# Kernel tuning notes

Hardware: AMD Instinct MI355X
Metric: run time of the kernel (lower is better)

Reference implementation:

```python
import jax, jax.numpy as jnp
import numpy as np

# Assumptions (helpers not included in source):
#  - drop_edge(A, 0.8, training) is identity at inference (training=False); we
#    implement the deterministic eval path.
#  - normalized_laplacian_tilde_matrix(A) = D~^{-1/2} (A + I) D~^{-1/2}, the
#    renormalization-trick adjacency (A_tilde = A + I, D~ = rowsum(A_tilde)).

def setup_inputs() -> dict:
    key = jax.random.key(0)
    kx, kA, kW = jax.random.split(key, 3)
    B, C, Co, T, N, K = 64, 64, 64, 32, 64, 3
    x = jax.random.normal(kx, (B, C, T, N), dtype=jnp.float32)
    A = jax.random.uniform(kA, (B, K, T, N, N), dtype=jnp.float32)
    W = jax.random.normal(kW, (Co, C), dtype=jnp.float32) * 0.02  # 1x1 conv weight
    b = jnp.zeros((Co,), dtype=jnp.float32)
    return {"x": x, "A": A, "W": W, "b": b}


def reference(x, A, W, b):
    # 1x1 Conv2d == per-position channel mixing
    x = jnp.einsum('bctn,oc->botn', x, W) + b[None, :, None, None]

    # Vectorized normalized-Laplacian-tilde over all (B, K, T) graphs at once.
    N = A.shape[-1]
    A_tilde = A + jnp.eye(N, dtype=A.dtype)            # (B,K,T,N,N)
    deg = jnp.sum(A_tilde, axis=-1)                    # (B,K,T,N)
    dinv = jax.lax.rsqrt(deg)                          # deg >= 1, safe
    A_norm = A_tilde * dinv[..., :, None] * dinv[..., None, :]

    # Per-(k,t) bmm: out[b,c,t,m] = sum_k sum_n x[b,c,t,n] * A_norm[b,k,t,n,m]
    x_out = jnp.einsum('bctn,bktnm->bctm', x, A_norm)
    return (x_out, A)
```

## Files before the change

### kernel.cpp

```cpp
#include <hip/hip_runtime.h>
#include <hip/hip_bf16.h>

typedef __attribute__((ext_vector_type(8))) short short8;
typedef __attribute__((ext_vector_type(4))) short short4v;
typedef __attribute__((ext_vector_type(4))) float f32x4;

#define Bb 64
#define Cc 64
#define Tt 32
#define Nn 64
#define Kk 3
#define PITCH 72
#define OUT_A_OFF 8388608L

__device__ __forceinline__ short f2bf(float f) {
    __hip_bfloat16 h = __float2bfloat16(f);
    return *reinterpret_cast<short*>(&h);
}

__global__ __launch_bounds__(256, 4) void ctg_kernel(
    const float* __restrict__ X,
    const float* __restrict__ A,
    const float* __restrict__ W,
    const float* __restrict__ bias,
    float* __restrict__ out)
{
    __shared__ short sW [Cc * PITCH];
    __shared__ short sXT[Nn * PITCH];
    __shared__ short sX1[Cc * PITCH];
    __shared__ short sAT[Nn * PITCH];
    __shared__ float sDinv[Nn];
    __shared__ float sB[Cc];

    const int tid = threadIdx.x;
    const int b = blockIdx.x >> 5;
    const int t = blockIdx.x & 31;
    const int l  = tid & 63;
    const int w  = tid >> 6;
    const int lr = l & 15;
    const int lq = l >> 4;

    const long xbase = (long)b * (Cc * Tt * Nn) + (long)t * Nn;

    #pragma unroll
    for (int j = 0; j < 4; ++j) {
        int q  = tid + 256 * j;
        int r  = q >> 4;
        int c0 = (q & 15) * 4;
        f32x4 wv = *(const f32x4*)(W + r * 64 + c0);
        short4v ws;
        #pragma unroll
        for (int i = 0; i < 4; ++i) ws[i] = f2bf(wv[i]);
        *(short4v*)&sW[r * PITCH + c0] = ws;
        f32x4 xv = *(const f32x4*)(X + xbase + (long)r * (Tt * Nn) + c0);
        #pragma unroll
        for (int i = 0; i < 4; ++i) sXT[(c0 + i) * PITCH + r] = f2bf(xv[i]);
    }
    if (tid < Cc) sB[tid] = bias[tid];
    __syncthreads();

    short8 aw0 = *(const short8*)&sW[(16 * w + lr) * PITCH + 8 * lq];
    short8 aw1 = *(const short8*)&sW[(16 * w + lr) * PITCH + 32 + 8 * lq];
    f32x4 acc1[4];
    #pragma unroll
    for (int nt = 0; nt < 4; ++nt) {
        acc1[nt] = (f32x4){0.f, 0.f, 0.f, 0.f};
        short8 b0 = *(const short8*)&sXT[(16 * nt + lr) * PITCH + 8 * lq];
        short8 b1 = *(const short8*)&sXT[(16 * nt + lr) * PITCH + 32 + 8 * lq];
        acc1[nt] = __builtin_amdgcn_mfma_f32_16x16x32_bf16(aw0, b0, acc1[nt], 0, 0, 0);
        acc1[nt] = __builtin_amdgcn_mfma_f32_16x16x32_bf16(aw1, b1, acc1[nt], 0, 0, 0);
    }
    #pragma unroll
    for (int nt = 0; nt < 4; ++nt)
        #pragma unroll
        for (int r = 0; r < 4; ++r) {
            int c = 16 * w + 4 * lq + r;
            sX1[c * PITCH + 16 * nt + lr] = f2bf(acc1[nt][r] + sB[c]);
        }

    f32x4 acc3[4];
    #pragma unroll
    for (int mt = 0; mt < 4; ++mt) acc3[mt] = (f32x4){0.f, 0.f, 0.f, 0.f};

    const int m0 = (tid & 15) * 4;
    const long Abase0 = (long)b * (Kk * Tt * Nn * Nn) + (long)t * (Nn * Nn);

    for (int k = 0; k < Kk; ++k) {
        __syncthreads();

        const long Ab = Abase0 + (long)k * (Tt * Nn * Nn);
        f32x4 av[4];
        #pragma unroll
        for (int e = 0; e < 4; ++e) av[e] = *(const f32x4*)(A + Ab + 4 * (tid + 256 * e));
        #pragma unroll
        for (int e = 0; e < 4; ++e) *(f32x4*)(out + OUT_A_OFF + Ab + 4 * (tid + 256 * e)) = av[e];

        float dg[4];
        #pragma unroll
        for (int e = 0; e < 4; ++e) {
            float q = av[e][0] + av[e][1] + av[e][2] + av[e][3];
            q += __shfl_xor(q, 1);
            q += __shfl_xor(q, 2);
            q += __shfl_xor(q, 4);
            q += __shfl_xor(q, 8);
            dg[e] = q;
        }
        if ((tid & 15) == 0) {
            #pragma unroll
            for (int e = 0; e < 4; ++e)
                sDinv[(tid >> 4) + 16 * e] = rsqrtf(dg[e] + 1.0f);
        }
        __syncthreads();

        float dm[4] = { sDinv[m0], sDinv[m0 + 1], sDinv[m0 + 2], sDinv[m0 + 3] };
        #pragma unroll
        for (int e = 0; e < 4; ++e) {
            int n = (tid >> 4) + 16 * e;
            float dn = sDinv[n];
            #pragma unroll
            for (int i = 0; i < 4; ++i) {
                float v = av[e][i];
                if (m0 + i == n) v += 1.0f;
                sAT[(m0 + i) * PITCH + n] = f2bf(v * dn * dm[i]);
            }
        }
        __syncthreads();

        short8 a0 = *(const short8*)&sX1[(16 * w + lr) * PITCH + 8 * lq];
        short8 a1 = *(const short8*)&sX1[(16 * w + lr) * PITCH + 32 + 8 * lq];
        #pragma unroll
        for (int mt = 0; mt < 4; ++mt) {
            short8 b0 = *(const short8*)&sAT[(16 * mt + lr) * PITCH + 8 * lq];
            short8 b1 = *(const short8*)&sAT[(16 * mt + lr) * PITCH + 32 + 8 * lq];
            acc3[mt] = __builtin_amdgcn_mfma_f32_16x16x32_bf16(a0, b0, acc3[mt], 0, 0, 0);
            acc3[mt] = __builtin_amdgcn_mfma_f32_16x16x32_bf16(a1, b1, acc3[mt], 0, 0, 0);
        }
    }

    #pragma unroll
    for (int mt = 0; mt < 4; ++mt)
        #pragma unroll
        for (int r = 0; r < 4; ++r) {
            int c = 16 * w + 4 * lq + r;
            out[xbase + (long)c * (Tt * Nn) + 16 * mt + lr] = acc3[mt][r];
        }
}

extern "C" void kernel_launch(void* const* d_in, const int* in_sizes, int n_in,
                              void* d_out, int out_size, void* d_ws, size_t ws_size,
                              hipStream_t stream) {
    const float* X    = (const float*)d_in[0];
    const float* A    = (const float*)d_in[1];
    const float* W    = (const float*)d_in[2];
    const float* bias = (const float*)d_in[3];
    float* out = (float*)d_out;
    ctg_kernel<<<dim3(Bb * Tt), dim3(256), 0, stream>>>(X, A, W, bias, out);
}
```

Before: 243.6 us.

## Prefetch next A slice, shrink shared memory for higher occupancy, use nontemporal stores

New measurement: 250.3 us. 1.03x slower.

```diff
diff --git a/kernel.cpp b/kernel.cpp
--- a/kernel.cpp
+++ b/kernel.cpp
@@ -2,7 +2,6 @@
 #include <hip/hip_bf16.h>
 
 typedef __attribute__((ext_vector_type(8))) short short8;
-typedef __attribute__((ext_vector_type(4))) short short4v;
 typedef __attribute__((ext_vector_type(4))) float f32x4;
 
 #define Bb 64
@@ -18,19 +17,16 @@
     return *reinterpret_cast<short*>(&h);
 }
 
-__global__ __launch_bounds__(256, 4) void ctg_kernel(
+__global__ __launch_bounds__(256, 8) void ctg_kernel(
     const float* __restrict__ X,
     const float* __restrict__ A,
     const float* __restrict__ W,
     const float* __restrict__ bias,
     float* __restrict__ out)
 {
-    __shared__ short sW [Cc * PITCH];
-    __shared__ short sXT[Nn * PITCH];
-    __shared__ short sX1[Cc * PITCH];
-    __shared__ short sAT[Nn * PITCH];
+    __shared__ __align__(16) short buf1[Nn * PITCH];
+    __shared__ __align__(16) short buf0[Nn * PITCH];
     __shared__ float sDinv[Nn];
-    __shared__ float sB[Cc];
 
     const int tid = threadIdx.x;
     const int b = blockIdx.x >> 5;
@@ -40,42 +36,56 @@
     const int lr = l & 15;
     const int lq = l >> 4;
 
-    const long xbase = (long)b * (Cc * Tt * Nn) + (long)t * Nn;
+    const long xbase  = (long)b * (Cc * Tt * Nn) + (long)t * Nn;
+    const long Abase0 = (long)b * (Kk * Tt * Nn * Nn) + (long)t * (Nn * Nn);
+    const float* Aptr = A + Abase0 + 4 * tid;
+
+    f32x4 av[4];
+    #pragma unroll
+    for (int e = 0; e < 4; ++e) av[e] = *(const f32x4*)(Aptr + 1024 * e);
 
     #pragma unroll
     for (int j = 0; j < 4; ++j) {
         int q  = tid + 256 * j;
         int r  = q >> 4;
         int c0 = (q & 15) * 4;
-        f32x4 wv = *(const f32x4*)(W + r * 64 + c0);
-        short4v ws;
-        #pragma unroll
-        for (int i = 0; i < 4; ++i) ws[i] = f2bf(wv[i]);
-        *(short4v*)&sW[r * PITCH + c0] = ws;
         f32x4 xv = *(const f32x4*)(X + xbase + (long)r * (Tt * Nn) + c0);
         #pragma unroll
-        for (int i = 0; i < 4; ++i) sXT[(c0 + i) * PITCH + r] = f2bf(xv[i]);
+        for (int i = 0; i < 4; ++i) buf1[(c0 + i) * PITCH + r] = f2bf(xv[i]);
     }
-    if (tid < Cc) sB[tid] = bias[tid];
+
+    const float* wrow = W + (16 * w + lr) * 64 + 8 * lq;
+    f32x4 w00 = *(const f32x4*)(wrow);
+    f32x4 w01 = *(const f32x4*)(wrow + 4);
+    f32x4 w10 = *(const f32x4*)(wrow + 32);
+    f32x4 w11 = *(const f32x4*)(wrow + 36);
+    short8 aw0, aw1;
+    #pragma unroll
+    for (int i = 0; i < 4; ++i) {
+        aw0[i] = f2bf(w00[i]); aw0[4 + i] = f2bf(w01[i]);
+        aw1[i] = f2bf(w10[i]); aw1[4 + i] = f2bf(w11[i]);
+    }
+    f32x4 bv = *(const f32x4*)(bias + 16 * w + 4 * lq);
+
     __syncthreads();
 
-    short8 aw0 = *(const short8*)&sW[(16 * w + lr) * PITCH + 8 * lq];
-    short8 aw1 = *(const short8*)&sW[(16 * w + lr) * PITCH + 32 + 8 * lq];
     f32x4 acc1[4];
     #pragma unroll
     for (int nt = 0; nt < 4; ++nt) {
         acc1[nt] = (f32x4){0.f, 0.f, 0.f, 0.f};
-        short8 b0 = *(const short8*)&sXT[(16 * nt + lr) * PITCH + 8 * lq];
-        short8 b1 = *(const short8*)&sXT[(16 * nt + lr) * PITCH + 32 + 8 * lq];
+        short8 b0 = *(const short8*)&buf1[(16 * nt + lr) * PITCH + 8 * lq];
+        short8 b1 = *(const short8*)&buf1[(16 * nt + lr) * PITCH + 32 + 8 * lq];
         acc1[nt] = __builtin_amdgcn_mfma_f32_16x16x32_bf16(aw0, b0, acc1[nt], 0, 0, 0);
         acc1[nt] = __builtin_amdgcn_mfma_f32_16x16x32_bf16(aw1, b1, acc1[nt], 0, 0, 0);
     }
+    __syncthreads();
+
     #pragma unroll
     for (int nt = 0; nt < 4; ++nt)
         #pragma unroll
         for (int r = 0; r < 4; ++r) {
             int c = 16 * w + 4 * lq + r;
-            sX1[c * PITCH + 16 * nt + lr] = f2bf(acc1[nt][r] + sB[c]);
+            buf1[c * PITCH + 16 * nt + lr] = f2bf(acc1[nt][r] + bv[r]);
         }
 
     f32x4 acc3[4];
@@ -83,19 +93,15 @@
     for (int mt = 0; mt < 4; ++mt) acc3[mt] = (f32x4){0.f, 0.f, 0.f, 0.f};
 
     const int m0 = (tid & 15) * 4;
-    const long Abase0 = (long)b * (Kk * Tt * Nn * Nn) + (long)t * (Nn * Nn);
+    const int nrow = tid >> 4;
 
     for (int k = 0; k < Kk; ++k) {
-        __syncthreads();
+        const long Ab = Abase0 + (long)k * (Tt * Nn * Nn);
 
-        const long Ab = Abase0 + (long)k * (Tt * Nn * Nn);
-        f32x4 av[4];
         #pragma unroll
-        for (int e = 0; e < 4; ++e) av[e] = *(const f32x4*)(A + Ab + 4 * (tid + 256 * e));
-        #pragma unroll
-        for (int e = 0; e < 4; ++e) *(f32x4*)(out + OUT_A_OFF + Ab + 4 * (tid + 256 * e)) = av[e];
+        for (int e = 0; e < 4; ++e)
+            __builtin_nontemporal_store(av[e], (f32x4*)(out + OUT_A_OFF + Ab + 4 * (tid + 256 * e)));
 
-        float dg[4];
         #pragma unroll
         for (int e = 0; e < 4; ++e) {
             float q = av[e][0] + av[e][1] + av[e][2] + av[e][3];
@@ -103,35 +109,36 @@
             q += __shfl_xor(q, 2);
             q += __shfl_xor(q, 4);
             q += __shfl_xor(q, 8);
-            dg[e] = q;
-        }
-        if ((tid & 15) == 0) {
-            #pragma unroll
-            for (int e = 0; e < 4; ++e)
-                sDinv[(tid >> 4) + 16 * e] = rsqrtf(dg[e] + 1.0f);
+            if ((tid & 15) == 0) sDinv[nrow + 16 * e] = rsqrtf(q + 1.0f);
         }
         __syncthreads();
 
         float dm[4] = { sDinv[m0], sDinv[m0 + 1], sDinv[m0 + 2], sDinv[m0 + 3] };
         #pragma unroll
         for (int e = 0; e < 4; ++e) {
-            int n = (tid >> 4) + 16 * e;
+            int n = nrow + 16 * e;
             float dn = sDinv[n];
             #pragma unroll
             for (int i = 0; i < 4; ++i) {
                 float v = av[e][i];
                 if (m0 + i == n) v += 1.0f;
-                sAT[(m0 + i) * PITCH + n] = f2bf(v * dn * dm[i]);
+                buf0[(m0 + i) * PITCH + n] = f2bf(v * dn * dm[i]);
             }
+        }
+
+        if (k + 1 < Kk) {
+            #pragma unroll
+            for (int e = 0; e < 4; ++e)
+                av[e] = *(const f32x4*)(Aptr + (k + 1) * (Tt * Nn * Nn) + 1024 * e);
         }
         __syncthreads();
 
-        short8 a0 = *(const short8*)&sX1[(16 * w + lr) * PITCH + 8 * lq];
-        short8 a1 = *(const short8*)&sX1[(16 * w + lr) * PITCH + 32 + 8 * lq];
+        short8 a0 = *(const short8*)&buf1[(16 * w + lr) * PITCH + 8 * lq];
+        short8 a1 = *(const short8*)&buf1[(16 * w + lr) * PITCH + 32 + 8 * lq];
         #pragma unroll
         for (int mt = 0; mt < 4; ++mt) {
-            short8 b0 = *(const short8*)&sAT[(16 * mt + lr) * PITCH + 8 * lq];
-            short8 b1 = *(const short8*)&sAT[(16 * mt + lr) * PITCH + 32 + 8 * lq];
+            short8 b0 = *(const short8*)&buf0[(16 * mt + lr) * PITCH + 8 * lq];
+            short8 b1 = *(const short8*)&buf0[(16 * mt + lr) * PITCH + 32 + 8 * lq];
             acc3[mt] = __builtin_amdgcn_mfma_f32_16x16x32_bf16(a0, b0, acc3[mt], 0, 0, 0);
             acc3[mt] = __builtin_amdgcn_mfma_f32_16x16x32_bf16(a1, b1, acc3[mt], 0, 0, 0);
         }
@@ -142,7 +149,8 @@
         #pragma unroll
         for (int r = 0; r < 4; ++r) {
             int c = 16 * w + 4 * lq + r;
-            out[xbase + (long)c * (Tt * Nn) + 16 * mt + lr] = acc3[mt][r];
+            __builtin_nontemporal_store(acc3[mt][r],
+                out + xbase + (long)c * (Tt * Nn) + 16 * mt + lr);
         }
 }
 
```
